# Performance work log

Hardware: AMD Instinct MI355X
Metric: run time of the kernel (lower is better)

Reference implementation:

```python
import jax, jax.numpy as jnp
import numpy as np

C = 1.0            # curvature args.c
EPS = 1e-7         # Hyperboloid eps for float32
MIN_NORM = 1e-15
MAX_SQDIST = 50.0
NUM_LAYERS = 3     # args.num_layers (resSumGCN hops)
MARGIN = 0.1       # args.margin
N_NODES = 200000
NUM_USERS = 100000
EMB_DIM = 64
E_ADJ = 1600000
E_TR = 65536
NUM_NEG = 16


def _mink_dot(x, y, keepdim=True):
    # Minkowski inner product: -x0*y0 + sum_i xi*yi
    res = jnp.sum(x * y, axis=-1) - 2.0 * x[..., 0] * y[..., 0]
    return res[..., None] if keepdim else res


def _sqdist(x, y, c):
    K = 1.0 / c
    prod = _mink_dot(x, y)                      # [E, 1]
    theta = jnp.maximum(-prod / K, 1.0 + EPS)
    return jnp.minimum(K * jnp.arccosh(theta) ** 2, MAX_SQDIST)


def _expmap0(u, c):
    sqrtK = (1.0 / c) ** 0.5
    x = u[..., 1:]
    x_norm = jnp.maximum(jnp.linalg.norm(x, axis=-1, keepdims=True), MIN_NORM)
    theta = x_norm / sqrtK
    first = sqrtK * jnp.cosh(theta)
    rest = sqrtK * jnp.sinh(theta) * x / x_norm
    return jnp.concatenate([first, rest], axis=-1)


def _logmap0(x, c):
    sqrtK = (1.0 / c) ** 0.5
    y = x[..., 1:]
    y_norm = jnp.maximum(jnp.linalg.norm(y, axis=-1, keepdims=True), MIN_NORM)
    theta = jnp.maximum(x[..., :1] / sqrtK, 1.0 + EPS)
    rest = sqrtK * jnp.arccosh(theta) * y / y_norm
    return jnp.concatenate([jnp.zeros_like(rest[..., :1]), rest], axis=-1)


def _proj(x, c):
    K = 1.0 / c
    y = x[..., 1:]
    first = jnp.sqrt(K + jnp.sum(y * y, axis=-1, keepdims=True))
    return jnp.concatenate([first, y], axis=-1)


def setup_inputs() -> dict:
    key = jax.random.key(0)
    ks = jax.random.split(key, 8)
    # embedding init: uniform(-scale, scale) tangent vector, then expmap0 onto hyperboloid
    tan = jax.random.uniform(ks[0], (N_NODES, EMB_DIM), minval=-0.1, maxval=0.1, dtype=jnp.float32)
    weight = _expmap0(tan, C)
    adj_row = jnp.sort(jax.random.randint(ks[1], (E_ADJ,), 0, N_NODES, dtype=jnp.int32))
    adj_col = jax.random.randint(ks[2], (E_ADJ,), 0, N_NODES, dtype=jnp.int32)
    # mimic symmetric-normalized adjacency values (~1/deg)
    adj_vals = jax.random.uniform(ks[3], (E_ADJ,), dtype=jnp.float32) * 0.125
    anchor = jax.random.randint(ks[4], (E_TR,), 0, NUM_USERS, dtype=jnp.int32)
    pos = jax.random.randint(ks[5], (E_TR,), 0, NUM_USERS, dtype=jnp.int32) + NUM_USERS
    neg = jax.random.randint(ks[6], (E_TR, NUM_NEG), 0, NUM_USERS, dtype=jnp.int32) + NUM_USERS
    return {"weight": weight, "adj_vals": adj_vals, "adj_row": adj_row,
            "adj_col": adj_col, "anchor": anchor, "pos": pos, "neg": neg}


def _encode(weight, adj_row, adj_col, adj_vals):
    # HypAgg: logmap0 -> resSumGCN (sum of adj^k x for k=1..L) -> expmap0 -> proj
    x_t = _logmap0(weight, C)
    h = x_t
    acc = jnp.zeros_like(x_t)
    for _ in range(NUM_LAYERS):
        h = jax.ops.segment_sum(adj_vals[:, None] * h[adj_col], adj_row,
                                num_segments=N_NODES, indices_are_sorted=True)
        acc = acc + h
    return _proj(_expmap0(acc, C), C)


def reference(weight, adj_vals, adj_row, adj_col, anchor, pos, neg):
    h = _encode(weight, adj_row, adj_col, adj_vals)      # [N, d] on hyperboloid
    emb_a = h[anchor]                                    # [E, d]
    emb_p = h[pos]                                       # [E, d]
    # decode_pos: sqdist + hratio weight
    pos_scores = _sqdist(emb_a, emb_p, C)                # [E, 1]
    u0 = emb_a[:, 0]
    i0 = emb_p[:, 0]
    score = (1.0 - _mink_dot(emb_a, emb_p, keepdim=False) - u0 - i0) / (u0 * i0)
    w = jax.nn.sigmoid(-score)[:, None]                  # [E, 1]
    # decode_neg: hard-negative mining (euclidean sqdist to positive, take min)
    d2 = jnp.sum((h[neg] - emb_p[:, None, :]) ** 2, axis=-1)   # [E, num_neg]
    hard_idx = jnp.argmin(d2, axis=1)
    hard_neg = jnp.take_along_axis(neg, hard_idx[:, None], axis=1)[:, 0]
    neg_scores = _sqdist(emb_a, h[hard_neg], C)          # [E, 1]
    # margin ranking loss with hyperbolic-ratio weight
    loss = jnp.sum(jnp.maximum(pos_scores - neg_scores + MARGIN * w, 0.0))
    return loss
```

## Files before the change

### kernel.cpp

```cpp
#include <hip/hip_runtime.h>
#include <hip/hip_bf16.h>
#include <math.h>

#define N_NODES 200000
#define EMB_DIM 64
#define E_ADJ 1600000
#define E_TR 65536
#define NUM_NEG 16
#define EPS 1e-7f
#define MIN_NORM 1e-15f
#define MAX_SQDIST 50.0f
#define MARGIN 0.1f
#define LOSS_BLOCKS (E_TR / 4)
#define SPMM_BLOCKS 2048
#define NWAVES (SPMM_BLOCKS * 4)
#define RPW 25
#define LDS_CAP 512

#define PACK_BLOCKS ((E_ADJ + 255) / 256)
#define RP_BLOCKS   ((N_NODES + 1 + 255) / 256)
#define LOG_BLOCKS  ((N_NODES + 15) / 16)

typedef float f4 __attribute__((ext_vector_type(4)));

__device__ __forceinline__ float group_reduce16(float v) {
    v += __shfl_xor(v, 8, 64);
    v += __shfl_xor(v, 4, 64);
    v += __shfl_xor(v, 2, 64);
    v += __shfl_xor(v, 1, 64);
    return v;
}

__device__ __forceinline__ float dot4(f4 a, f4 b) {
    return a.x * b.x + a.y * b.y + a.z * b.z + a.w * b.w;
}

__device__ __forceinline__ unsigned bfr(float f) {
    unsigned u = __float_as_uint(f);
    return (u + 0x7fffu + ((u >> 16) & 1u)) >> 16;
}
__device__ __forceinline__ uint2 f42bf(f4 v) {
    return make_uint2(bfr(v.x) | (bfr(v.y) << 16), bfr(v.z) | (bfr(v.w) << 16));
}
__device__ __forceinline__ f4 bf2f4(uint2 g) {
    f4 r;
    r.x = __uint_as_float(g.x << 16);
    r.y = __uint_as_float(g.x & 0xffff0000u);
    r.z = __uint_as_float(g.y << 16);
    r.w = __uint_as_float(g.y & 0xffff0000u);
    return r;
}

__global__ void prelude_kernel(const int* __restrict__ cols, const float* __restrict__ vals,
                               int2* __restrict__ ev, const int* __restrict__ rows,
                               int* __restrict__ rp, const float* __restrict__ w,
                               uint2* __restrict__ xt) {
    int b = blockIdx.x;
    if (b < PACK_BLOCKS) {
        int i = b * 256 + threadIdx.x;
        if (i < E_ADJ) ev[i] = make_int2(cols[i] << 4, __float_as_int(vals[i]));
    } else if (b < PACK_BLOCKS + RP_BLOCKS) {
        int r = (b - PACK_BLOCKS) * 256 + threadIdx.x;
        if (r <= N_NODES) {
            int lo = 0, hi = E_ADJ;
            while (lo < hi) {
                int mid = (lo + hi) >> 1;
                if (rows[mid] < r) lo = mid + 1; else hi = mid;
            }
            rp[r] = lo;
        }
    } else {
        int bb = b - PACK_BLOCKS - RP_BLOCKS;
        int wave = bb * 4 + (threadIdx.x >> 6);
        int lane = threadIdx.x & 63;
        int e = lane >> 4, d = lane & 15;
        int node = wave * 4 + e;
        if (node < N_NODES) {
            f4 v = ((const f4*)w)[(node << 4) + d];
            f4 y = v;
            if (d == 0) y.x = 0.0f;
            float n2 = group_reduce16(dot4(y, y));
            float ynorm = fmaxf(sqrtf(n2), MIN_NORM);
            float w0 = __shfl(v.x, lane & 48, 64);
            float theta = fmaxf(w0, 1.0f + EPS);
            float scale = acoshf(theta) / ynorm;
            xt[(node << 4) + d] = f42bf(y * scale);
        }
    }
}

__device__ __forceinline__ f4 spmm_row_lds(const uint2* __restrict__ h_in,
                                           const int2* __restrict__ ev,
                                           const int2* L, int ebase, int staged,
                                           int s, int re, int e, int d) {
    f4 acc = {0.f, 0.f, 0.f, 0.f};
    int i = s;
    for (; i + 8 <= re; i += 8) {
        int2 cv0, cv1;
        if (i + 8 - ebase <= staged) {
            cv0 = L[i - ebase + e];
            cv1 = L[i - ebase + 4 + e];
        } else {
            cv0 = ev[i + e];
            cv1 = ev[i + 4 + e];
        }
        uint2 g0 = h_in[cv0.x + d];
        uint2 g1 = h_in[cv1.x + d];
        acc += bf2f4(g0) * __int_as_float(cv0.y);
        acc += bf2f4(g1) * __int_as_float(cv1.y);
    }
    if (i + 4 <= re) {
        int2 cv;
        if (i + 4 - ebase <= staged) cv = L[i - ebase + e];
        else                         cv = ev[i + e];
        uint2 g = h_in[cv.x + d];
        acc += bf2f4(g) * __int_as_float(cv.y);
        i += 4;
    }
    if (i + e < re) {
        int2 cv;
        if (re - ebase <= staged) cv = L[i - ebase + e];
        else                      cv = ev[i + e];
        uint2 g = h_in[cv.x + d];
        acc += bf2f4(g) * __int_as_float(cv.y);
    }
    acc.x += __shfl_xor(acc.x, 16, 64); acc.y += __shfl_xor(acc.y, 16, 64);
    acc.z += __shfl_xor(acc.z, 16, 64); acc.w += __shfl_xor(acc.w, 16, 64);
    acc.x += __shfl_xor(acc.x, 32, 64); acc.y += __shfl_xor(acc.y, 32, 64);
    acc.z += __shfl_xor(acc.z, 32, 64); acc.w += __shfl_xor(acc.w, 32, 64);
    return acc;
}

__global__ __launch_bounds__(256) void spmm_kernel(const uint2* __restrict__ h_in,
                                                   uint2* __restrict__ h_out,
                                                   const int2* __restrict__ ev,
                                                   const int* __restrict__ rp) {
    __shared__ int2 evs[4][LDS_CAP];
    int wib = threadIdx.x >> 6;
    int lane = threadIdx.x & 63;
    int e = lane >> 4, d = lane & 15;
    int wid = __builtin_amdgcn_readfirstlane(blockIdx.x * 4 + wib);
    int r0 = wid * RPW;
    if (r0 >= N_NODES) return;
    int r1 = min(r0 + RPW, N_NODES);
    int ebase = rp[r0];
    int etot  = rp[r1];
    int staged = min(etot - ebase, LDS_CAP);
    int2* L = evs[wib];
    for (int k = lane; k < staged; k += 64)
        L[k] = ev[ebase + k];
    __syncthreads();

    int s = ebase;
    int re = rp[r0 + 1];
    for (int row = r0; row < r1; ++row) {
        int re_next = (row + 1 < r1) ? rp[row + 2] : 0;
        f4 acc = spmm_row_lds(h_in, ev, L, ebase, staged, s, re, e, d);
        if (e == 0)
            h_out[(row << 4) + d] = f42bf(acc);
        s = re; re = re_next;
    }
}

__global__ __launch_bounds__(256) void spmm_expmap_kernel(const uint2* __restrict__ h_gather,
                                                          const uint2* __restrict__ h1,
                                                          const uint2* __restrict__ h2,
                                                          float* __restrict__ h,
                                                          float* __restrict__ nrm2,
                                                          const int2* __restrict__ ev,
                                                          const int* __restrict__ rp) {
    __shared__ int2 evs[4][LDS_CAP];
    int wib = threadIdx.x >> 6;
    int lane = threadIdx.x & 63;
    int e = lane >> 4, d = lane & 15;
    int wid = __builtin_amdgcn_readfirstlane(blockIdx.x * 4 + wib);
    int r0 = wid * RPW;
    if (r0 >= N_NODES) return;
    int r1 = min(r0 + RPW, N_NODES);
    int ebase = rp[r0];
    int etot  = rp[r1];
    int staged = min(etot - ebase, LDS_CAP);
    int2* L = evs[wib];
    for (int k = lane; k < staged; k += 64)
        L[k] = ev[ebase + k];
    __syncthreads();

    int s = ebase;
    int re = rp[r0 + 1];
    for (int row = r0; row < r1; ++row) {
        int re_next = (row + 1 < r1) ? rp[row + 2] : 0;
        int oi = (row << 4) + d;
        f4 a1 = bf2f4(h1[oi]);
        f4 a2 = bf2f4(h2[oi]);
        f4 acc = spmm_row_lds(h_gather, ev, L, ebase, staged, s, re, e, d);
        f4 u = (a1 + a2) + acc;
        f4 x = u;
        if (d == 0) x.x = 0.0f;
        float n2 = group_reduce16(dot4(x, x));
        float xn = fmaxf(sqrtf(n2), MIN_NORM);
        float sh = sinhf(xn);
        f4 rest = x * (sh / xn);
        float r2 = group_reduce16(dot4(rest, rest));
        float first = sqrtf(1.0f + r2);
        f4 ov = rest;
        if (d == 0) ov.x = first;
        if (e == 0) {
            ((f4*)h)[oi] = ov;
            if (d == 0) nrm2[row] = first * first + r2;
        }
        s = re; re = re_next;
    }
}

__global__ void loss_kernel(const float* __restrict__ h, const float* __restrict__ nrm2,
                            const int* __restrict__ anchor, const int* __restrict__ pos,
                            const int* __restrict__ neg, float* __restrict__ partials) {
    int wib = threadIdx.x >> 6;
    int lane = threadIdx.x & 63;
    int e = lane >> 4, d = lane & 15;
    int i = __builtin_amdgcn_readfirstlane(blockIdx.x * 4 + wib);
    const f4* H = (const f4*)h;

    int ia = anchor[i], ip = pos[i];
    f4 a4 = H[(ia << 4) + d];
    f4 p4 = H[(ip << 4) + d];
    int4 nb4 = ((const int4*)(neg + (size_t)i * NUM_NEG))[e];

    float s[4];
    s[0] = dot4(p4, H[(nb4.x << 4) + d]);
    s[1] = dot4(p4, H[(nb4.y << 4) + d]);
    s[2] = dot4(p4, H[(nb4.z << 4) + d]);
    s[3] = dot4(p4, H[(nb4.w << 4) + d]);
    float dap = dot4(a4, p4);

    {
        bool hi = (d & 8) != 0;
        float send0 = hi ? s[0] : s[2];
        float send1 = hi ? s[1] : s[3];
        float r0 = __shfl_xor(send0, 8, 64);
        float r1 = __shfl_xor(send1, 8, 64);
        float k0 = hi ? s[2] : s[0];
        float k1 = hi ? s[3] : s[1];
        s[0] = k0 + r0;
        s[1] = k1 + r1;
    }
    float sv;
    {
        bool hi = (d & 4) != 0;
        float send = hi ? s[0] : s[1];
        float r = __shfl_xor(send, 4, 64);
        float k = hi ? s[1] : s[0];
        sv = k + r;
    }
    sv += __shfl_xor(sv, 2, 64);
    sv += __shfl_xor(sv, 1, 64);
    int b_lane = ((d >> 3) & 1) * 2 + ((d >> 2) & 1);
    int nidx_lane = (d & 8) ? ((d & 4) ? nb4.w : nb4.z)
                            : ((d & 4) ? nb4.y : nb4.x);
    int j_lane = 4 * e + b_lane;

    float np2 = nrm2[ip];
    float bd = nrm2[nidx_lane] + np2 - 2.0f * sv;
    int bj = j_lane;
    #pragma unroll
    for (int off = 32; off > 0; off >>= 1) {
        float od = __shfl_xor(bd, off, 64);
        int   oj = __shfl_xor(bj, off, 64);
        if (od < bd || (od == bd && oj < bj)) { bd = od; bj = oj; }
    }
    int bn = neg[(size_t)i * NUM_NEG + __builtin_amdgcn_readfirstlane(bj)];
    f4 w4 = H[(bn << 4) + d];
    float dan = group_reduce16(dot4(a4, w4));
    dap = group_reduce16(dap);

    float loss = 0.0f;
    if (lane == 0) {
        float a0 = a4.x, p0 = p4.x, n0 = w4.x;
        float mink = dap - 2.0f * a0 * p0;
        float th = fmaxf(-mink, 1.0f + EPS);
        float ac = acoshf(th);
        float pos_score = fminf(ac * ac, MAX_SQDIST);
        float score = (1.0f - mink - a0 - p0) / (a0 * p0);
        float wgt = 1.0f / (1.0f + expf(score));
        float minkn = dan - 2.0f * a0 * n0;
        float thn = fmaxf(-minkn, 1.0f + EPS);
        float acn = acoshf(thn);
        float neg_score = fminf(acn * acn, MAX_SQDIST);
        loss = fmaxf(pos_score - neg_score + MARGIN * wgt, 0.0f);
    }
    __shared__ float part[4];
    if (lane == 0) part[wib] = loss;
    __syncthreads();
    if (threadIdx.x == 0)
        partials[blockIdx.x] = part[0] + part[1] + part[2] + part[3];
}

__global__ void reduce_kernel(const float* __restrict__ partials, float* __restrict__ out) {
    int tid = threadIdx.x;
    float s = 0.0f;
    for (int i = tid; i < LOSS_BLOCKS; i += 1024)
        s += partials[i];
    #pragma unroll
    for (int off = 32; off > 0; off >>= 1)
        s += __shfl_xor(s, off, 64);
    __shared__ float part[16];
    if ((tid & 63) == 0) part[tid >> 6] = s;
    __syncthreads();
    if (tid == 0) {
        float t = 0.0f;
        #pragma unroll
        for (int k = 0; k < 16; ++k) t += part[k];
        out[0] = t;
    }
}

extern "C" void kernel_launch(void* const* d_in, const int* in_sizes, int n_in,
                              void* d_out, int out_size, void* d_ws, size_t ws_size,
                              hipStream_t stream) {
    const float* weight   = (const float*)d_in[0];
    const float* adj_vals = (const float*)d_in[1];
    const int*   adj_row  = (const int*)d_in[2];
    const int*   adj_col  = (const int*)d_in[3];
    const int*   anchor   = (const int*)d_in[4];
    const int*   pos      = (const int*)d_in[5];
    const int*   neg      = (const int*)d_in[6];
    float* out = (float*)d_out;

    const size_t NODEF32 = (size_t)N_NODES * EMB_DIM * sizeof(float);
    const size_t NODEBF  = (size_t)N_NODES * EMB_DIM * sizeof(unsigned short);
    const size_t MB = 1024 * 1024;
    char* ws = (char*)d_ws;
    float* hfin = (float*)(ws);
    uint2* bf0  = (uint2*)(ws + NODEF32);
    uint2* bf1  = (uint2*)(ws + NODEF32 + NODEBF);
    uint2* bf2  = (uint2*)(ws + NODEF32 + 2 * NODEBF);
    int*   rp   = (int*)  (ws + NODEF32 + 3 * NODEBF);
    float* nrm2 = (float*)(ws + NODEF32 + 3 * NODEBF + 1 * MB);
    int2*  ev   = (int2*) (ws + NODEF32 + 3 * NODEBF + 2 * MB);
    float* partials = (float*)(ws + NODEF32 + 3 * NODEBF + 16 * MB);

    prelude_kernel<<<PACK_BLOCKS + RP_BLOCKS + LOG_BLOCKS, 256, 0, stream>>>(
        adj_col, adj_vals, ev, adj_row, rp, weight, bf0);
    spmm_kernel<<<SPMM_BLOCKS, 256, 0, stream>>>(bf0, bf1, ev, rp);
    spmm_kernel<<<SPMM_BLOCKS, 256, 0, stream>>>(bf1, bf2, ev, rp);
    spmm_expmap_kernel<<<SPMM_BLOCKS, 256, 0, stream>>>(bf2, bf1, bf2, hfin, nrm2, ev, rp);
    loss_kernel<<<LOSS_BLOCKS, 256, 0, stream>>>(hfin, nrm2, anchor, pos, neg, partials);
    reduce_kernel<<<1, 1024, 0, stream>>>(partials, out);
}
```

Measured before the change: 353.2 us.

## Assign one row per 16-lane group in SpMM instead of splitting edges

The SpMM kernels change their work split. Before, the four 16-lane groups of a wave each took a different edge of the same row and were combined with cross-group shuffles. Now each group handles its own row and walks that row's edges serially, unrolled by two, so the shuffle reduction and the per-row serial loop go away. The cost is divergence when row lengths differ within a wave, and group_reduce16 is now called inside a divergent `valid` branch, which risks correctness if that helper relies on full-wave shuffles.

```diff
diff --git a/kernel.cpp b/kernel.cpp
--- a/kernel.cpp
+++ b/kernel.cpp
@@ -89,45 +89,29 @@
     }
 }
 
-__device__ __forceinline__ f4 spmm_row_lds(const uint2* __restrict__ h_in,
-                                           const int2* __restrict__ ev,
-                                           const int2* L, int ebase, int staged,
-                                           int s, int re, int e, int d) {
+__device__ __forceinline__ f4 row_accum(const uint2* __restrict__ h_in,
+                                        const int2* __restrict__ ev,
+                                        const int2* L, int ebase, int staged,
+                                        int s, int e, int d) {
     f4 acc = {0.f, 0.f, 0.f, 0.f};
-    int i = s;
-    for (; i + 8 <= re; i += 8) {
+    int k = s;
+    for (; k + 2 <= e; k += 2) {
+        int o0 = k - ebase;
         int2 cv0, cv1;
-        if (i + 8 - ebase <= staged) {
-            cv0 = L[i - ebase + e];
-            cv1 = L[i - ebase + 4 + e];
-        } else {
-            cv0 = ev[i + e];
-            cv1 = ev[i + 4 + e];
-        }
+        if (o0 + 1 < staged) { cv0 = L[o0]; cv1 = L[o0 + 1]; }
+        else                 { cv0 = ev[k]; cv1 = ev[k + 1]; }
         uint2 g0 = h_in[cv0.x + d];
         uint2 g1 = h_in[cv1.x + d];
         acc += bf2f4(g0) * __int_as_float(cv0.y);
         acc += bf2f4(g1) * __int_as_float(cv1.y);
     }
-    if (i + 4 <= re) {
+    if (k < e) {
+        int o = k - ebase;
         int2 cv;
-        if (i + 4 - ebase <= staged) cv = L[i - ebase + e];
-        else                         cv = ev[i + e];
-        uint2 g = h_in[cv.x + d];
-        acc += bf2f4(g) * __int_as_float(cv.y);
-        i += 4;
-    }
-    if (i + e < re) {
-        int2 cv;
-        if (re - ebase <= staged) cv = L[i - ebase + e];
-        else                      cv = ev[i + e];
-        uint2 g = h_in[cv.x + d];
-        acc += bf2f4(g) * __int_as_float(cv.y);
-    }
-    acc.x += __shfl_xor(acc.x, 16, 64); acc.y += __shfl_xor(acc.y, 16, 64);
-    acc.z += __shfl_xor(acc.z, 16, 64); acc.w += __shfl_xor(acc.w, 16, 64);
-    acc.x += __shfl_xor(acc.x, 32, 64); acc.y += __shfl_xor(acc.y, 32, 64);
-    acc.z += __shfl_xor(acc.z, 32, 64); acc.w += __shfl_xor(acc.w, 32, 64);
+        if (o < staged) cv = L[o]; else cv = ev[k];
+        uint2 gg = h_in[cv.x + d];
+        acc += bf2f4(gg) * __int_as_float(cv.y);
+    }
     return acc;
 }
 
@@ -138,7 +122,7 @@
     __shared__ int2 evs[4][LDS_CAP];
     int wib = threadIdx.x >> 6;
     int lane = threadIdx.x & 63;
-    int e = lane >> 4, d = lane & 15;
+    int g = lane >> 4, d = lane & 15;
     int wid = __builtin_amdgcn_readfirstlane(blockIdx.x * 4 + wib);
     int r0 = wid * RPW;
     if (r0 >= N_NODES) return;
@@ -151,14 +135,14 @@
         L[k] = ev[ebase + k];
     __syncthreads();
 
-    int s = ebase;
-    int re = rp[r0 + 1];
-    for (int row = r0; row < r1; ++row) {
-        int re_next = (row + 1 < r1) ? rp[row + 2] : 0;
-        f4 acc = spmm_row_lds(h_in, ev, L, ebase, staged, s, re, e, d);
-        if (e == 0)
+    for (int base = r0; base < r1; base += 4) {
+        int row = base + g;
+        bool valid = row < r1;
+        int s = 0, e = 0;
+        if (valid) { s = rp[row]; e = rp[row + 1]; }
+        f4 acc = row_accum(h_in, ev, L, ebase, staged, s, e, d);
+        if (valid)
             h_out[(row << 4) + d] = f42bf(acc);
-        s = re; re = re_next;
     }
 }
 
@@ -172,7 +156,7 @@
     __shared__ int2 evs[4][LDS_CAP];
     int wib = threadIdx.x >> 6;
     int lane = threadIdx.x & 63;
-    int e = lane >> 4, d = lane & 15;
+    int g = lane >> 4, d = lane & 15;
     int wid = __builtin_amdgcn_readfirstlane(blockIdx.x * 4 + wib);
     int r0 = wid * RPW;
     if (r0 >= N_NODES) return;
@@ -185,30 +169,33 @@
         L[k] = ev[ebase + k];
     __syncthreads();
 
-    int s = ebase;
-    int re = rp[r0 + 1];
-    for (int row = r0; row < r1; ++row) {
-        int re_next = (row + 1 < r1) ? rp[row + 2] : 0;
+    for (int base = r0; base < r1; base += 4) {
+        int row = base + g;
+        bool valid = row < r1;
+        int s = 0, e = 0;
         int oi = (row << 4) + d;
-        f4 a1 = bf2f4(h1[oi]);
-        f4 a2 = bf2f4(h2[oi]);
-        f4 acc = spmm_row_lds(h_gather, ev, L, ebase, staged, s, re, e, d);
-        f4 u = (a1 + a2) + acc;
-        f4 x = u;
-        if (d == 0) x.x = 0.0f;
-        float n2 = group_reduce16(dot4(x, x));
-        float xn = fmaxf(sqrtf(n2), MIN_NORM);
-        float sh = sinhf(xn);
-        f4 rest = x * (sh / xn);
-        float r2 = group_reduce16(dot4(rest, rest));
-        float first = sqrtf(1.0f + r2);
-        f4 ov = rest;
-        if (d == 0) ov.x = first;
-        if (e == 0) {
+        f4 a1 = {0.f,0.f,0.f,0.f}, a2 = {0.f,0.f,0.f,0.f};
+        if (valid) {
+            s = rp[row]; e = rp[row + 1];
+            a1 = bf2f4(h1[oi]);
+            a2 = bf2f4(h2[oi]);
+        }
+        f4 acc = row_accum(h_gather, ev, L, ebase, staged, s, e, d);
+        if (valid) {
+            f4 u = (a1 + a2) + acc;
+            f4 x = u;
+            if (d == 0) x.x = 0.0f;
+            float n2 = group_reduce16(dot4(x, x));
+            float xn = fmaxf(sqrtf(n2), MIN_NORM);
+            float sh = sinhf(xn);
+            f4 rest = x * (sh / xn);
+            float r2 = group_reduce16(dot4(rest, rest));
+            float first = sqrtf(1.0f + r2);
+            f4 ov = rest;
+            if (d == 0) ov.x = first;
             ((f4*)h)[oi] = ov;
             if (d == 0) nrm2[row] = first * first + r2;
         }
-        s = re; re = re_next;
     }
 }
 
```

Result: faster. 333.7 us (-5.5%).
